# Optimization experiments

Measured on AMD Instinct MI355X. Metric: run time of the kernel, lower is better.

## Reference

```python
import jax, jax.numpy as jnp
import numpy as np

EPS = 1e-8


def quaternion_mul(q, m):
    # Hamilton product q * m over last dim of size 4 (w, x, y, z)
    w1, x1, y1, z1 = q[..., 0], q[..., 1], q[..., 2], q[..., 3]
    w2, x2, y2, z2 = m[..., 0], m[..., 1], m[..., 2], m[..., 3]
    return jnp.stack([
        w1 * w2 - x1 * x2 - y1 * y2 - z1 * z2,
        w1 * x2 + x1 * w2 + y1 * z2 - z1 * y2,
        w1 * y2 - x1 * z2 + y1 * w2 + z1 * x2,
        w1 * z2 + x1 * y2 - y1 * x2 + z1 * w2,
    ], axis=-1)


def quaternion_normalize(q):
    n = jnp.linalg.norm(q, axis=-1, keepdims=True)
    return q / (n + EPS)


def setup_inputs() -> dict:
    key = jax.random.key(0)
    k = jax.random.split(key, 5)
    B, S, D, H = 4, 2048, 1024, 1024
    scale = 0.02
    return {
        "x": jax.random.normal(k[0], (B, S, D), dtype=jnp.float32),
        "W_in": jax.random.normal(k[1], (3 * H, D), dtype=jnp.float32) * scale,
        "b_in": jax.random.normal(k[2], (3 * H,), dtype=jnp.float32) * scale,
        "W_out": jax.random.normal(k[3], (D, 4 * H), dtype=jnp.float32) * scale,
        "b_out": jax.random.normal(k[4], (D,), dtype=jnp.float32) * scale,
    }


def reference(x, W_in, b_in, W_out, b_out):
    B, S, D = x.shape
    H = W_in.shape[0] // 3
    # input projection -> rotation parameters v in R^3 per hidden channel
    v = (jnp.einsum('bsd,ed->bse', x, W_in) + b_in).reshape(B, S, H, 3)
    # SU(2) exponential map: v -> unit quaternion
    theta = jnp.linalg.norm(v, axis=-1, keepdims=True)          # (B,S,H,1)
    axis = v / (theta + EPS)
    q_inputs = jnp.concatenate([jnp.cos(theta), jnp.sin(theta) * axis], axis=-1)  # (B,S,H,4)

    # initial identity quaternion state (B,H,4)
    m0 = jnp.zeros((B, H, 4), dtype=x.dtype).at[..., 0].set(1.0)

    def step(m, q_t):
        m_new = quaternion_normalize(quaternion_mul(q_t, m))
        return m_new, m_new

    q_seq = jnp.transpose(q_inputs, (1, 0, 2, 3))               # (S,B,H,4)
    m_final, ms = jax.lax.scan(step, m0, q_seq)                 # ms: (S,B,H,4)

    states = jnp.transpose(ms, (1, 0, 2, 3)).reshape(B, S, 4 * H)
    full_output = jnp.einsum('bsf,df->bsd', states, W_out) + b_out
    return full_output, m_final
```

## Files before the change

kernel.cpp:

```cpp
#include <hip/hip_runtime.h>
#include <hip/hip_bf16.h>
#include <stdint.h>

#define EPSF 1e-8f

typedef __attribute__((ext_vector_type(8))) short short8;
typedef __attribute__((ext_vector_type(8))) _Float16 half8;
typedef __attribute__((ext_vector_type(16))) float floatx16;

__device__ __forceinline__ unsigned short f2h(float f) {
    _Float16 h = (_Float16)f;
    return __builtin_bit_cast(unsigned short, h);
}
__device__ __forceinline__ float h2f(unsigned short u) {
    return (float)__builtin_bit_cast(_Float16, u);
}


__global__ void prep_kernel(const float4* __restrict__ x4, ushort4* __restrict__ x16,
                            const float4* __restrict__ wi4, ushort4* __restrict__ wi16,
                            const float4* __restrict__ wo4, ushort4* __restrict__ wo16,
                            int nx4, int nw4, int nwo4) {
    int i = blockIdx.x * blockDim.x + threadIdx.x;
    float4 f; ushort4 u;
    if (i < nx4) {
        f = x4[i];
        u.x = f2h(f.x); u.y = f2h(f.y); u.z = f2h(f.z); u.w = f2h(f.w);
        x16[i] = u;
    } else if (i < nx4 + nw4) {
        int j = i - nx4;
        f = wi4[j];
        u.x = f2h(f.x); u.y = f2h(f.y); u.z = f2h(f.z); u.w = f2h(f.w);
        wi16[j] = u;
    } else if (i < nx4 + nw4 + nwo4) {
        int j = i - nx4 - nw4;
        f = wo4[j];
        u.x = f2h(f.x); u.y = f2h(f.y); u.z = f2h(f.z); u.w = f2h(f.w);
        wo16[j] = u;
    }
}


__device__ __forceinline__ void gld16(const unsigned short* g, unsigned short* l) {
    __builtin_amdgcn_global_load_lds(
        (const __attribute__((address_space(1))) unsigned int*)g,
        (__attribute__((address_space(3))) unsigned int*)l, 16, 0, 0);
}

template <int BM, int BN, int BK, bool HALFOUT>
__global__ __launch_bounds__(256)
void gemm_bt(const unsigned short* __restrict__ Am, const unsigned short* __restrict__ Bm,
             const float* __restrict__ bias, void* __restrict__ Cv,
             int M, int N, int K) {
    constexpr int IF  = BM / 64;
    constexpr int JF  = BN / 64;
    constexpr int KH  = BK / 16;
    constexpr int CPR = BK / 8;
    extern __shared__ unsigned short smem[];
    unsigned short* sA = smem;
    unsigned short* sB = smem + BM * BK;

    const int tid  = threadIdx.x;
    const int lane = tid & 63;
    const int wid  = tid >> 6;
    const int wr   = wid >> 1, wc = wid & 1;
    const int m32  = lane & 31, half = lane >> 5;

    const int rowA0 = blockIdx.y * BM;
    const int rowB0 = blockIdx.x * BN;

    floatx16 acc[IF][JF];
#pragma unroll
    for (int i = 0; i < IF; i++)
#pragma unroll
        for (int j = 0; j < JF; j++)
#pragma unroll
            for (int r = 0; r < 16; r++) acc[i][j][r] = 0.f;

    const int nk = K / BK;
    for (int kt = 0; kt < nk; ++kt) {
        const int k0 = kt * BK;
#pragma unroll
        for (int i = 0; i < BM * CPR / 256; i++) {
            int c = tid + 256 * i;
            int r = c / CPR, ccl = c % CPR;
            int ccg = ccl ^ (r & (CPR - 1));
            gld16(Am + (size_t)(rowA0 + r) * K + k0 + ccg * 8, sA + c * 8);
        }
#pragma unroll
        for (int i = 0; i < BN * CPR / 256; i++) {
            int c = tid + 256 * i;
            int r = c / CPR, ccl = c % CPR;
            int ccg = ccl ^ (r & (CPR - 1));
            gld16(Bm + (size_t)(rowB0 + r) * K + k0 + ccg * 8, sB + c * 8);
        }
        __syncthreads();

#pragma unroll
        for (int kh = 0; kh < KH; kh++) {
            const int kc = kh * 2 + half;
            short8 a[IF], b[JF];
#pragma unroll
            for (int i = 0; i < IF; i++) {
                int ra = wr * (BM / 2) + i * 32 + m32;
                int pa = ra * CPR + (kc ^ (ra & (CPR - 1)));
                a[i] = *(const short8*)(sA + pa * 8);
            }
#pragma unroll
            for (int j = 0; j < JF; j++) {
                int rb = wc * (BN / 2) + j * 32 + m32;
                int pb = rb * CPR + (kc ^ (rb & (CPR - 1)));
                b[j] = *(const short8*)(sB + pb * 8);
            }
#pragma unroll
            for (int i = 0; i < IF; i++)
#pragma unroll
                for (int j = 0; j < JF; j++)
                    acc[i][j] = __builtin_amdgcn_mfma_f32_32x32x16_f16(
                        __builtin_bit_cast(half8, a[i]), __builtin_bit_cast(half8, b[j]),
                        acc[i][j], 0, 0, 0);
        }
        __syncthreads();
    }

#pragma unroll
    for (int i = 0; i < IF; i++) {
#pragma unroll
        for (int j = 0; j < JF; j++) {
            int col  = rowB0 + wc * (BN / 2) + j * 32 + m32;
            float bv = bias[col];
#pragma unroll
            for (int r = 0; r < 16; r++) {
                int row = rowA0 + wr * (BM / 2) + i * 32 + (r & 3) + 8 * (r >> 2) + 4 * half;
                if (HALFOUT)
                    ((unsigned short*)Cv)[(size_t)row * N + col] = f2h(acc[i][j][r] + bv);
                else
                    ((float*)Cv)[(size_t)row * N + col] = acc[i][j][r] + bv;
            }
        }
    }
}


struct Q { float w, x, y, z; };

__device__ __forceinline__ Q qmul(Q a, Q b) {
    Q r;
    r.w = a.w * b.w - a.x * b.x - a.y * b.y - a.z * b.z;
    r.x = a.w * b.x + a.x * b.w + a.y * b.z - a.z * b.y;
    r.y = a.w * b.y - a.x * b.z + a.y * b.w + a.z * b.x;
    r.z = a.w * b.z + a.x * b.y - a.y * b.x + a.z * b.w;
    return r;
}
__device__ __forceinline__ Q qnorm(Q a) {
    float nn = a.w * a.w + a.x * a.x + a.y * a.y + a.z * a.z;
    float inv = __frsqrt_rn(nn);
    Q r; r.w = a.w * inv; r.x = a.x * inv; r.y = a.y * inv; r.z = a.z * inv;
    return r;
}
__device__ __forceinline__ Q vquat(float vx, float vy, float vz) {
    float th = sqrtf(vx * vx + vy * vy + vz * vz);
    float s_, c_;
    __sincosf(th, &s_, &c_);
    float k = __fdividef(s_, th + EPSF);
    Q q; q.w = c_; q.x = k * vx; q.y = k * vy; q.z = k * vz;
    return q;
}

#define SEG  64
#define NSEG 32

__global__ __launch_bounds__(256)
void seg_prod_kernel(const unsigned short* __restrict__ v, float* __restrict__ partials,
                     int S, int H) {
    const int b  = blockIdx.z;
    const int h  = blockIdx.y * 64 + (threadIdx.x & 63);
    const int sg = blockIdx.x * 4 + (threadIdx.x >> 6);
    const int s0 = sg * SEG;
    const size_t vstep = (size_t)3 * H;
    const unsigned short* vp = v + ((size_t)b * S + s0) * vstep + (size_t)h * 3;

    constexpr int CH = 8;
    float ax[CH], ay[CH], az[CH], bx[CH], by[CH], bz[CH];
#pragma unroll
    for (int i = 0; i < CH; ++i) {
        ax[i] = h2f(vp[i * vstep + 0]); ay[i] = h2f(vp[i * vstep + 1]); az[i] = h2f(vp[i * vstep + 2]);
    }
    Q c = {1.f, 0.f, 0.f, 0.f};
    const int NC = SEG / CH;
    for (int cc = 0; cc < NC; cc += 2) {
        if (cc + 1 < NC) {
            const unsigned short* p = vp + (size_t)(cc + 1) * CH * vstep;
#pragma unroll
            for (int i = 0; i < CH; ++i) {
                bx[i] = h2f(p[i * vstep + 0]); by[i] = h2f(p[i * vstep + 1]); bz[i] = h2f(p[i * vstep + 2]);
            }
        }
#pragma unroll
        for (int i = 0; i < CH; ++i) c = qmul(vquat(ax[i], ay[i], az[i]), c);
        if (cc + 2 < NC) {
            const unsigned short* p = vp + (size_t)(cc + 2) * CH * vstep;
#pragma unroll
            for (int i = 0; i < CH; ++i) {
                ax[i] = h2f(p[i * vstep + 0]); ay[i] = h2f(p[i * vstep + 1]); az[i] = h2f(p[i * vstep + 2]);
            }
        }
#pragma unroll
        for (int i = 0; i < CH; ++i) c = qmul(vquat(bx[i], by[i], bz[i]), c);
    }
    float4* dst = (float4*)(partials + (((size_t)b * NSEG + sg) * H + h) * 4);
    *dst = make_float4(c.w, c.x, c.y, c.z);
}

__global__ __launch_bounds__(256)
void apply_kernel(const unsigned short* __restrict__ v, const float* __restrict__ partials,
                  unsigned short* __restrict__ st, float* __restrict__ m_final,
                  int S, int H) {
    const int b   = blockIdx.z;
    const int hb  = blockIdx.y * 64;
    const int hl  = threadIdx.x & 63;
    const int h   = hb + hl;
    const int sg  = blockIdx.x * 4 + (threadIdx.x >> 6);
    const int s0  = sg * SEG;
    const size_t vstep = (size_t)3 * H;
    const size_t sstep = (size_t)4 * H;
    const unsigned short* vp = v + ((size_t)b * S + s0) * vstep + (size_t)h * 3;
    unsigned short* sp = st + ((size_t)b * S + s0) * sstep + (size_t)h * 4;

    __shared__ float4 lp[NSEG][64];
    for (int i = threadIdx.x; i < NSEG * 64; i += 256) {
        int s2 = i >> 6, hh = i & 63;
        lp[s2][hh] = *(const float4*)(partials + (((size_t)b * NSEG + s2) * H + hb + hh) * 4);
    }
    __syncthreads();

    Q R = {1.f, 0.f, 0.f, 0.f};
    for (int s2 = 0; s2 < sg; ++s2) {
        float4 pv = lp[s2][hl];
        Q pq = {pv.x, pv.y, pv.z, pv.w};
        R = qmul(pq, R);
    }

    constexpr int CH = 8;
    float ax[CH], ay[CH], az[CH], bx[CH], by[CH], bz[CH];
#pragma unroll
    for (int i = 0; i < CH; ++i) {
        ax[i] = h2f(vp[i * vstep + 0]); ay[i] = h2f(vp[i * vstep + 1]); az[i] = h2f(vp[i * vstep + 2]);
    }
    const int NC = SEG / CH;
    for (int cc = 0; cc < NC; cc += 2) {
        if (cc + 1 < NC) {
            const unsigned short* pp = vp + (size_t)(cc + 1) * CH * vstep;
#pragma unroll
            for (int i = 0; i < CH; ++i) {
                bx[i] = h2f(pp[i * vstep + 0]); by[i] = h2f(pp[i * vstep + 1]); bz[i] = h2f(pp[i * vstep + 2]);
            }
        }
#pragma unroll
        for (int i = 0; i < CH; ++i) {
            R = qmul(vquat(ax[i], ay[i], az[i]), R);
            Q m = qnorm(R);
            ushort4 u; u.x = f2h(m.w); u.y = f2h(m.x); u.z = f2h(m.y); u.w = f2h(m.z);
            *(ushort4*)(sp + (size_t)(cc * CH + i) * sstep) = u;
        }
        if (cc + 2 < NC) {
            const unsigned short* pp = vp + (size_t)(cc + 2) * CH * vstep;
#pragma unroll
            for (int i = 0; i < CH; ++i) {
                ax[i] = h2f(pp[i * vstep + 0]); ay[i] = h2f(pp[i * vstep + 1]); az[i] = h2f(pp[i * vstep + 2]);
            }
        }
#pragma unroll
        for (int i = 0; i < CH; ++i) {
            R = qmul(vquat(bx[i], by[i], bz[i]), R);
            Q m = qnorm(R);
            ushort4 u; u.x = f2h(m.w); u.y = f2h(m.x); u.z = f2h(m.y); u.w = f2h(m.z);
            *(ushort4*)(sp + (size_t)((cc + 1) * CH + i) * sstep) = u;
        }
    }

    if (sg == NSEG - 1) {
        Q m = qnorm(R);
        float* mf = m_final + ((size_t)b * H + h) * 4;
        mf[0] = m.w; mf[1] = m.x; mf[2] = m.y; mf[3] = m.z;
    }
}


extern "C" void kernel_launch(void* const* d_in, const int* in_sizes, int n_in,
                              void* d_out, int out_size, void* d_ws, size_t ws_size,
                              hipStream_t stream) {
    const float* x     = (const float*)d_in[0];
    const float* W_in  = (const float*)d_in[1];
    const float* b_in  = (const float*)d_in[2];
    const float* W_out = (const float*)d_in[3];
    const float* b_out = (const float*)d_in[4];
    float* out = (float*)d_out;

    const int B = 4, S = 2048, D = 1024, H = 1024;
    const int M  = B * S;
    const int N1 = 3 * H;
    const int K1 = D;
    const int N2 = D;
    const int K2 = 4 * H;

    char* ws = (char*)d_ws;
    unsigned short* v    = (unsigned short*)(ws);
    unsigned short* st   = (unsigned short*)(ws + 50331648u);
    unsigned short* x16  = (unsigned short*)(ws + 50331648u);
    unsigned short* wi16 = (unsigned short*)(ws + 50331648u + 16777216u);
    unsigned short* wo16 = (unsigned short*)(ws + 117440512u);

    float* partials = out;

    const int nx  = M * K1;
    const int nw  = N1 * K1;
    const int nwo = N2 * K2;
    const int n4  = (nx + nw + nwo) / 4;

    prep_kernel<<<(n4 + 255) / 256, 256, 0, stream>>>(
        (const float4*)x, (ushort4*)x16, (const float4*)W_in, (ushort4*)wi16,
        (const float4*)W_out, (ushort4*)wo16, nx / 4, nw / 4, nwo / 4);

    gemm_bt<128, 128, 64, true><<<dim3(N1 / 128, M / 128), 256, 32768, stream>>>(
        x16, wi16, b_in, v, M, N1, K1);

    dim3 sg_grid(NSEG / 4, H / 64, B);
    seg_prod_kernel<<<sg_grid, 256, 0, stream>>>(v, partials, S, H);
    apply_kernel<<<sg_grid, 256, 0, stream>>>(v, partials, st, out + (size_t)M * D, S, H);

    gemm_bt<128, 128, 128, false><<<dim3(N2 / 128, M / 128), 256, 65536, stream>>>(
        st, wo16, b_out, out, M, N2, K2);
}
```

Baseline: 313.3 us.

## Fuse segmented quaternion scan into one kernel and retile output GEMM

After: 366.5 us. 17.0% more time.

```diff
diff --git a/kernel.cpp b/kernel.cpp
--- a/kernel.cpp
+++ b/kernel.cpp
@@ -47,13 +47,14 @@
         (__attribute__((address_space(3))) unsigned int*)l, 16, 0, 0);
 }
 
-template <int BM, int BN, int BK, bool HALFOUT>
-__global__ __launch_bounds__(256)
+template <int BM, int BN, int BK, bool HALFOUT, int NW_R, int NW_C>
+__global__ __launch_bounds__(NW_R * NW_C * 64)
 void gemm_bt(const unsigned short* __restrict__ Am, const unsigned short* __restrict__ Bm,
              const float* __restrict__ bias, void* __restrict__ Cv,
              int M, int N, int K) {
-    constexpr int IF  = BM / 64;
-    constexpr int JF  = BN / 64;
+    constexpr int NT  = NW_R * NW_C * 64;
+    constexpr int IF  = BM / (NW_R * 32);
+    constexpr int JF  = BN / (NW_C * 32);
     constexpr int KH  = BK / 16;
     constexpr int CPR = BK / 8;
     extern __shared__ unsigned short smem[];
@@ -63,7 +64,7 @@
     const int tid  = threadIdx.x;
     const int lane = tid & 63;
     const int wid  = tid >> 6;
-    const int wr   = wid >> 1, wc = wid & 1;
+    const int wr   = wid % NW_R, wc = wid / NW_R;
     const int m32  = lane & 31, half = lane >> 5;
 
     const int rowA0 = blockIdx.y * BM;
@@ -81,15 +82,15 @@
     for (int kt = 0; kt < nk; ++kt) {
         const int k0 = kt * BK;
 #pragma unroll
-        for (int i = 0; i < BM * CPR / 256; i++) {
-            int c = tid + 256 * i;
+        for (int i = 0; i < BM * CPR / NT; i++) {
+            int c = tid + NT * i;
             int r = c / CPR, ccl = c % CPR;
             int ccg = ccl ^ (r & (CPR - 1));
             gld16(Am + (size_t)(rowA0 + r) * K + k0 + ccg * 8, sA + c * 8);
         }
 #pragma unroll
-        for (int i = 0; i < BN * CPR / 256; i++) {
-            int c = tid + 256 * i;
+        for (int i = 0; i < BN * CPR / NT; i++) {
+            int c = tid + NT * i;
             int r = c / CPR, ccl = c % CPR;
             int ccg = ccl ^ (r & (CPR - 1));
             gld16(Bm + (size_t)(rowB0 + r) * K + k0 + ccg * 8, sB + c * 8);
@@ -102,13 +103,13 @@
             short8 a[IF], b[JF];
 #pragma unroll
             for (int i = 0; i < IF; i++) {
-                int ra = wr * (BM / 2) + i * 32 + m32;
+                int ra = wr * (BM / NW_R) + i * 32 + m32;
                 int pa = ra * CPR + (kc ^ (ra & (CPR - 1)));
                 a[i] = *(const short8*)(sA + pa * 8);
             }
 #pragma unroll
             for (int j = 0; j < JF; j++) {
-                int rb = wc * (BN / 2) + j * 32 + m32;
+                int rb = wc * (BN / NW_C) + j * 32 + m32;
                 int pb = rb * CPR + (kc ^ (rb & (CPR - 1)));
                 b[j] = *(const short8*)(sB + pb * 8);
             }
@@ -127,11 +128,11 @@
     for (int i = 0; i < IF; i++) {
 #pragma unroll
         for (int j = 0; j < JF; j++) {
-            int col  = rowB0 + wc * (BN / 2) + j * 32 + m32;
+            int col  = rowB0 + wc * (BN / NW_C) + j * 32 + m32;
             float bv = bias[col];
 #pragma unroll
             for (int r = 0; r < 16; r++) {
-                int row = rowA0 + wr * (BM / 2) + i * 32 + (r & 3) + 8 * (r >> 2) + 4 * half;
+                int row = rowA0 + wr * (BM / NW_R) + i * 32 + (r & 3) + 8 * (r >> 2) + 4 * half;
                 if (HALFOUT)
                     ((unsigned short*)Cv)[(size_t)row * N + col] = f2h(acc[i][j][r] + bv);
                 else
@@ -171,17 +172,22 @@
 #define NSEG 32
 
 __global__ __launch_bounds__(256)
-void seg_prod_kernel(const unsigned short* __restrict__ v, float* __restrict__ partials,
-                     int S, int H) {
-    const int b  = blockIdx.z;
-    const int h  = blockIdx.y * 64 + (threadIdx.x & 63);
-    const int sg = blockIdx.x * 4 + (threadIdx.x >> 6);
+void scan_kernel(const unsigned short* __restrict__ v, unsigned short* __restrict__ st,
+                 float* __restrict__ m_final, int S, int H) {
+    const int b  = blockIdx.y;
+    const int hb = blockIdx.x * 8;
+    const int hl = threadIdx.x & 7;
+    const int sg = threadIdx.x >> 3;
+    const int h  = hb + hl;
     const int s0 = sg * SEG;
     const size_t vstep = (size_t)3 * H;
+    const size_t sstep = (size_t)4 * H;
     const unsigned short* vp = v + ((size_t)b * S + s0) * vstep + (size_t)h * 3;
+    unsigned short* sp = st + ((size_t)b * S + s0) * sstep + (size_t)h * 4;
 
     constexpr int CH = 8;
     float ax[CH], ay[CH], az[CH], bx[CH], by[CH], bz[CH];
+
 #pragma unroll
     for (int i = 0; i < CH; ++i) {
         ax[i] = h2f(vp[i * vstep + 0]); ay[i] = h2f(vp[i * vstep + 1]); az[i] = h2f(vp[i * vstep + 2]);
@@ -208,46 +214,32 @@
 #pragma unroll
         for (int i = 0; i < CH; ++i) c = qmul(vquat(bx[i], by[i], bz[i]), c);
     }
-    float4* dst = (float4*)(partials + (((size_t)b * NSEG + sg) * H + h) * 4);
-    *dst = make_float4(c.w, c.x, c.y, c.z);
-}
-
-__global__ __launch_bounds__(256)
-void apply_kernel(const unsigned short* __restrict__ v, const float* __restrict__ partials,
-                  unsigned short* __restrict__ st, float* __restrict__ m_final,
-                  int S, int H) {
-    const int b   = blockIdx.z;
-    const int hb  = blockIdx.y * 64;
-    const int hl  = threadIdx.x & 63;
-    const int h   = hb + hl;
-    const int sg  = blockIdx.x * 4 + (threadIdx.x >> 6);
-    const int s0  = sg * SEG;
-    const size_t vstep = (size_t)3 * H;
-    const size_t sstep = (size_t)4 * H;
-    const unsigned short* vp = v + ((size_t)b * S + s0) * vstep + (size_t)h * 3;
-    unsigned short* sp = st + ((size_t)b * S + s0) * sstep + (size_t)h * 4;
-
-    __shared__ float4 lp[NSEG][64];
-    for (int i = threadIdx.x; i < NSEG * 64; i += 256) {
-        int s2 = i >> 6, hh = i & 63;
-        lp[s2][hh] = *(const float4*)(partials + (((size_t)b * NSEG + s2) * H + hb + hh) * 4);
-    }
+
+    __shared__ float4 prods[NSEG][8];
+    prods[sg][hl] = make_float4(c.w, c.x, c.y, c.z);
     __syncthreads();
 
-    Q R = {1.f, 0.f, 0.f, 0.f};
-    for (int s2 = 0; s2 < sg; ++s2) {
-        float4 pv = lp[s2][hl];
-        Q pq = {pv.x, pv.y, pv.z, pv.w};
-        R = qmul(pq, R);
-    }
-
-    constexpr int CH = 8;
-    float ax[CH], ay[CH], az[CH], bx[CH], by[CH], bz[CH];
+    if (threadIdx.x < 8) {
+        Q r = {1.f, 0.f, 0.f, 0.f};
+        for (int s2 = 0; s2 < NSEG; ++s2) {
+            float4 pv = prods[s2][threadIdx.x];
+            prods[s2][threadIdx.x] = make_float4(r.w, r.x, r.y, r.z);
+            Q pq = {pv.x, pv.y, pv.z, pv.w};
+            r = qmul(pq, r);
+        }
+        Q m = qnorm(r);
+        float* mf = m_final + ((size_t)b * H + hb + threadIdx.x) * 4;
+        mf[0] = m.w; mf[1] = m.x; mf[2] = m.y; mf[3] = m.z;
+    }
+    __syncthreads();
+
+    float4 e = prods[sg][hl];
+    Q R = {e.x, e.y, e.z, e.w};
+
 #pragma unroll
     for (int i = 0; i < CH; ++i) {
         ax[i] = h2f(vp[i * vstep + 0]); ay[i] = h2f(vp[i * vstep + 1]); az[i] = h2f(vp[i * vstep + 2]);
     }
-    const int NC = SEG / CH;
     for (int cc = 0; cc < NC; cc += 2) {
         if (cc + 1 < NC) {
             const unsigned short* pp = vp + (size_t)(cc + 1) * CH * vstep;
@@ -277,12 +269,6 @@
             ushort4 u; u.x = f2h(m.w); u.y = f2h(m.x); u.z = f2h(m.y); u.w = f2h(m.z);
             *(ushort4*)(sp + (size_t)((cc + 1) * CH + i) * sstep) = u;
         }
-    }
-
-    if (sg == NSEG - 1) {
-        Q m = qnorm(R);
-        float* mf = m_final + ((size_t)b * H + h) * 4;
-        mf[0] = m.w; mf[1] = m.x; mf[2] = m.y; mf[3] = m.z;
     }
 }
 
@@ -311,8 +297,6 @@
     unsigned short* wi16 = (unsigned short*)(ws + 50331648u + 16777216u);
     unsigned short* wo16 = (unsigned short*)(ws + 117440512u);
 
-    float* partials = out;
-
     const int nx  = M * K1;
     const int nw  = N1 * K1;
     const int nwo = N2 * K2;
@@ -322,13 +306,11 @@
         (const float4*)x, (ushort4*)x16, (const float4*)W_in, (ushort4*)wi16,
         (const float4*)W_out, (ushort4*)wo16, nx / 4, nw / 4, nwo / 4);
 
-    gemm_bt<128, 128, 64, true><<<dim3(N1 / 128, M / 128), 256, 32768, stream>>>(
+    gemm_bt<128, 128, 64, true, 2, 2><<<dim3(N1 / 128, M / 128), 256, 32768, stream>>>(
         x16, wi16, b_in, v, M, N1, K1);
 
-    dim3 sg_grid(NSEG / 4, H / 64, B);
-    seg_prod_kernel<<<sg_grid, 256, 0, stream>>>(v, partials, S, H);
-    apply_kernel<<<sg_grid, 256, 0, stream>>>(v, partials, st, out + (size_t)M * D, S, H);
-
-    gemm_bt<128, 128, 128, false><<<dim3(N2 / 128, M / 128), 256, 65536, stream>>>(
+    scan_kernel<<<dim3(H / 8, B), 256, 0, stream>>>(v, st, out + (size_t)M * D, S, H);
+
+    gemm_bt<128, 256, 64, false, 4, 2><<<dim3(N2 / 256, M / 128), 512, 49152, stream>>>(
         st, wo16, b_out, out, M, N2, K2);
 }
```
